# Kernel optimization log

Measured on AMD Instinct MI355X. Metric: run time of the kernel, lower is better.

Reference implementation:

```python
import jax, jax.numpy as jnp
import numpy as np

N_NODES = 100000
N_EDGES = 3200000
D_FEAT = 256
UNITS = 256


def setup_inputs() -> dict:
    key = jax.random.key(0)
    k1, k2, k3, k4, k5 = jax.random.split(key, 5)
    X = jax.random.normal(k1, (N_NODES, D_FEAT), dtype=jnp.float32)
    edge_row = jax.random.randint(k2, (N_EDGES,), 0, N_NODES, dtype=jnp.int64 if jax.config.read('jax_enable_x64') else jnp.int32)
    edge_col = jax.random.randint(k3, (N_EDGES,), 0, N_NODES, dtype=edge_row.dtype)
    edge_val = jax.random.uniform(k4, (N_EDGES,), dtype=jnp.float32)
    W = jax.random.normal(k5, (D_FEAT, UNITS), dtype=jnp.float32) * (1.0 / np.sqrt(D_FEAT))
    b = jnp.zeros((UNITS,), dtype=jnp.float32)
    return {"X": X, "edge_row": edge_row, "edge_col": edge_col,
            "edge_val": edge_val, "W": W, "b": b}


def reference(X, edge_row, edge_col, edge_val, W, b):
    # h = X @ W  (dense GEMM)  [N, units]
    h = X @ W
    # out = A @ h (sparse COO SpMM): out[i] = sum_e val[e] * h[col[e]] for row[e]==i
    msgs = edge_val[:, None] * h[edge_col]          # [E, units] gather + scale
    out = jax.ops.segment_sum(msgs, edge_row, num_segments=X.shape[0])
    out = out + b                                    # bias_add
    return jax.nn.relu(out)                          # activation
```

## Files before the change

kernel.cpp:

```cpp
#include <hip/hip_runtime.h>
#include <hip/hip_bf16.h>

#define N_NODES 100000
#define N_EDGES 3200000
#define D_FEAT  256
#define UNITS   256

#define BROWS   128
#define NB      782
#define NCHUNK  512
#define EPB     (N_EDGES / NCHUNK)
#define MAXB    6144
#define KPT     (MAXB / 512)
#define GEMMB   ((N_NODES + 127) / 128)

using frag_ab = __attribute__((ext_vector_type(8))) short;
using frag_cd = __attribute__((ext_vector_type(4))) float;

__device__ __forceinline__ unsigned short f2bf(float f) {
    union { float f; unsigned int i; } c; c.f = f;
    unsigned int r = c.i + 0x7FFF + ((c.i >> 16) & 1);
    return (unsigned short)(r >> 16);
}

__global__ __launch_bounds__(256) void convert_wt(const float* __restrict__ W,
                                                  unsigned short* __restrict__ Wt) {
    const int n = blockIdx.x, k = threadIdx.x;
    Wt[n * 256 + k] = f2bf(W[k * 256 + n]);
}

__global__ __launch_bounds__(512) void gemm_hist(const float* __restrict__ X,
                                                 const unsigned short* __restrict__ Wt,
                                                 unsigned char* __restrict__ hq,
                                                 float* __restrict__ hscale,
                                                 const int* __restrict__ erow,
                                                 int* __restrict__ hist_g) {
    __shared__ __align__(16) unsigned char smem[32768];
    __shared__ int rowmax_i[128];
    const int t = threadIdx.x;

    if (blockIdx.x >= GEMMB) {
        int* h = (int*)smem;
        const int b = blockIdx.x - GEMMB;
        for (int i = t; i < NB; i += 512) h[i] = 0;
        __syncthreads();
        const int base_e = b * EPB;
        for (int i = t; i < EPB; i += 512)
            atomicAdd(&h[erow[base_e + i] >> 7], 1);
        __syncthreads();
        for (int i = t; i < NB; i += 512)
            hist_g[b * NB + i] = h[i];
        return;
    }

    unsigned short* As = (unsigned short*)smem;
    unsigned short* Bs = (unsigned short*)(smem + 8192);
    unsigned char*  qbuf = smem;

    const int lane = t & 63;
    const int wave = t >> 6;
    const int wm   = (wave >> 2) * 64;
    const int wn   = (wave & 3) * 64;
    const int rowBase = blockIdx.x * 128;
    const int lr = lane & 15, lq = lane >> 4;

    if (t < 128) rowmax_i[t] = 0;

    frag_cd acc[4][4];
    #pragma unroll
    for (int i = 0; i < 4; ++i)
        #pragma unroll
        for (int j = 0; j < 4; ++j)
            acc[i][j] = (frag_cd){0.f, 0.f, 0.f, 0.f};

    for (int k0 = 0; k0 < D_FEAT; k0 += 32) {
        #pragma unroll
        for (int cc = 0; cc < 2; ++cc) {
            const int c = t + cc * 512;
            const int r = c >> 3, fo = (c & 7) * 4;
            const int grow = min(rowBase + r, N_NODES - 1);
            const float4 xv = *(const float4*)(X + (size_t)grow * D_FEAT + k0 + fo);
            ushort4 o;
            o.x = f2bf(xv.x); o.y = f2bf(xv.y); o.z = f2bf(xv.z); o.w = f2bf(xv.w);
            *(ushort4*)(As + r * 32 + fo) = o;
        }
        #pragma unroll
        for (int cc = 0; cc < 2; ++cc) {
            const int c = t + cc * 512;
            *(uint4*)(Bs + c * 8) =
                *(const uint4*)(Wt + (size_t)(c >> 2) * 256 + k0 + (c & 3) * 8);
        }
        __syncthreads();

        frag_ab a[4], b[4];
        #pragma unroll
        for (int i = 0; i < 4; ++i)
            a[i] = *(const frag_ab*)(As + (wm + i * 16 + lr) * 32 + lq * 8);
        #pragma unroll
        for (int j = 0; j < 4; ++j)
            b[j] = *(const frag_ab*)(Bs + (wn + j * 16 + lr) * 32 + lq * 8);

        #pragma unroll
        for (int i = 0; i < 4; ++i)
            #pragma unroll
            for (int j = 0; j < 4; ++j)
                acc[i][j] = __builtin_amdgcn_mfma_f32_16x16x32_bf16(
                    a[i], b[j], acc[i][j], 0, 0, 0);
        __syncthreads();
    }

    float pm[4][4];
    #pragma unroll
    for (int i = 0; i < 4; ++i)
        #pragma unroll
        for (int rr = 0; rr < 4; ++rr) {
            float m = fabsf(acc[i][0][rr]);
            m = fmaxf(m, fabsf(acc[i][1][rr]));
            m = fmaxf(m, fabsf(acc[i][2][rr]));
            m = fmaxf(m, fabsf(acc[i][3][rr]));
            pm[i][rr] = m;
        }
    #pragma unroll
    for (int o = 1; o <= 8; o <<= 1)
        #pragma unroll
        for (int i = 0; i < 4; ++i)
            #pragma unroll
            for (int rr = 0; rr < 4; ++rr)
                pm[i][rr] = fmaxf(pm[i][rr], __shfl_xor(pm[i][rr], o));
    if (lr == 0) {
        #pragma unroll
        for (int i = 0; i < 4; ++i)
            #pragma unroll
            for (int rr = 0; rr < 4; ++rr)
                atomicMax(&rowmax_i[wm + i * 16 + lq * 4 + rr],
                          __float_as_int(pm[i][rr]));
    }
    __syncthreads();

    #pragma unroll
    for (int i = 0; i < 4; ++i)
        #pragma unroll
        for (int rr = 0; rr < 4; ++rr) {
            const int row = wm + i * 16 + lq * 4 + rr;
            const float m = __int_as_float(rowmax_i[row]);
            const float inv = (m > 0.f) ? 127.f / m : 0.f;
            #pragma unroll
            for (int j = 0; j < 4; ++j) {
                const int q = (int)rintf(acc[i][j][rr] * inv);
                qbuf[row * 256 + wn + j * 16 + lr] = (unsigned char)(signed char)q;
            }
        }
    __syncthreads();

    #pragma unroll
    for (int cc = 0; cc < 4; ++cc) {
        const int c = t + cc * 512;
        const int row = c >> 4, fo = (c & 15) * 16;
        const int grow = rowBase + row;
        if (grow < N_NODES)
            *(uint4*)(hq + (size_t)grow * 256 + fo) = *(const uint4*)(qbuf + row * 256 + fo);
    }
    if (t < 128 && rowBase + t < N_NODES)
        hscale[rowBase + t] = __int_as_float(rowmax_i[t]) * (1.f / 127.f);
}

__global__ __launch_bounds__(512) void scan_buckets(const int* __restrict__ hist_g,
                                                    int* __restrict__ cum,
                                                    int* __restrict__ total) {
    const int k = blockIdx.x, t = threadIdx.x;
    __shared__ int p[512];
    const int v = hist_g[t * NB + k];
    p[t] = v;
    __syncthreads();
    for (int d = 1; d < 512; d <<= 1) {
        const int u = (t >= d) ? p[t - d] : 0;
        __syncthreads();
        p[t] += u;
        __syncthreads();
    }
    cum[t * NB + k] = p[t] - v;
    if (t == 511) total[k] = p[511];
}

__global__ __launch_bounds__(1024) void scan_base(const int* __restrict__ total,
                                                  int* __restrict__ base) {
    const int t = threadIdx.x;
    __shared__ int p[1024];
    const int v = (t < NB) ? total[t] : 0;
    p[t] = v;
    __syncthreads();
    for (int d = 1; d < 1024; d <<= 1) {
        const int u = (t >= d) ? p[t - d] : 0;
        __syncthreads();
        p[t] += u;
        __syncthreads();
    }
    if (t < NB) base[t] = p[t] - v;
    if (t == NB - 1) base[NB] = p[t];
}

__global__ __launch_bounds__(512) void scatter_binned(const int* __restrict__ erow,
                                                      const int* __restrict__ ecol,
                                                      const float* __restrict__ eval,
                                                      const float* __restrict__ hscale,
                                                      const int* __restrict__ cum,
                                                      const int* __restrict__ base,
                                                      uint2* __restrict__ binned) {
    __shared__ int cur[NB];
    const int t = threadIdx.x;
    const int b = blockIdx.x;
    for (int i = t; i < NB; i += 512)
        cur[i] = base[i] + cum[b * NB + i];
    __syncthreads();
    const int base_e = b * EPB;
    for (int i = t; i < EPB; i += 512) {
        const int e = base_e + i;
        const int r = erow[e];
        const int c = ecol[e];
        const float v = eval[e] * hscale[c];
        const int k = r >> 7, rl = r & 127;
        const int pos = atomicAdd(&cur[k], 1);
        binned[pos] = make_uint2(((unsigned)rl << 17) | (unsigned)c,
                                 __float_as_uint(v));
    }
}

__global__ __launch_bounds__(512) void sort_local(const uint2* __restrict__ binned,
                                                  const int* __restrict__ base,
                                                  const int* __restrict__ total,
                                                  uint2* __restrict__ sorted,
                                                  int* __restrict__ offs) {
    __shared__ uint2 buf[MAXB];
    __shared__ int lh[BROWS], loff[BROWS], lcur[BROWS];
    const int k = blockIdx.x, t = threadIdx.x;
    const int s = base[k];
    const int cnt = min(total[k], MAXB);

    uint2 ed[KPT];
    #pragma unroll
    for (int kk = 0; kk < KPT; ++kk) {
        const int i = t + kk * 512;
        if (i < cnt) ed[kk] = binned[s + i];
    }

    if (t < BROWS) lh[t] = 0;
    __syncthreads();
    #pragma unroll
    for (int kk = 0; kk < KPT; ++kk)
        if (t + kk * 512 < cnt)
            atomicAdd(&lh[ed[kk].x >> 17], 1);
    __syncthreads();
    if (t < BROWS) loff[t] = lh[t];
    __syncthreads();
    for (int d = 1; d < BROWS; d <<= 1) {
        const int u = (t >= d && t < BROWS) ? loff[t - d] : 0;
        __syncthreads();
        if (t < BROWS) loff[t] += u;
        __syncthreads();
    }
    if (t < BROWS) lcur[t] = loff[t] - lh[t];
    __syncthreads();
    #pragma unroll
    for (int kk = 0; kk < KPT; ++kk) {
        if (t + kk * 512 < cnt) {
            const int rl = ed[kk].x >> 17;
            const int p = atomicAdd(&lcur[rl], 1);
            buf[p] = make_uint2(ed[kk].x & 0x1FFFF, ed[kk].y);
        }
    }
    __syncthreads();
    for (int i = t; i < cnt; i += 512)
        sorted[s + i] = buf[i];
    const int rowBase = k * BROWS;
    if (t < BROWS && rowBase + t < N_NODES)
        offs[rowBase + t] = s + (loff[t] - lh[t]);
    if (t == 0 && k == NB - 1)
        offs[N_NODES] = N_EDGES;
}

__global__ __launch_bounds__(64) void spmm_rows(const int* __restrict__ offs,
                                                const uint2* __restrict__ sorted,
                                                const unsigned char* __restrict__ hq,
                                                const float* __restrict__ bias,
                                                float* __restrict__ out) {
    const int r = blockIdx.x;
    const int lane = threadIdx.x;
    __shared__ uint2 le[64];
    int s = offs[r];
    const int e = offs[r + 1];
    float a0 = 0.f, a1 = 0.f, a2 = 0.f, a3 = 0.f;

    while (s < e) {
        const int cnt = min(64, e - s);
        if (lane < cnt) {
            uint2 v = sorted[s + lane];
            v.x &= 0x1FFFF;
            le[lane] = v;
        }
        __syncthreads();
        #pragma unroll 4
        for (int j = 0; j < cnt; ++j) {
            const uint2 cv = le[j];
            const float v = __uint_as_float(cv.y);
            const unsigned int w = *(const unsigned int*)(hq + (size_t)cv.x * 256 + lane * 4);
            a0 += v * (float)((int)(signed char)( w        & 0xFF));
            a1 += v * (float)((int)(signed char)((w >> 8)  & 0xFF));
            a2 += v * (float)((int)(signed char)((w >> 16) & 0xFF));
            a3 += v * (float)((int)(signed char)( w >> 24        ));
        }
        __syncthreads();
        s += cnt;
    }

    const float4 b4 = *(const float4*)(bias + lane * 4);
    float4 o;
    o.x = fmaxf(a0 + b4.x, 0.f);
    o.y = fmaxf(a1 + b4.y, 0.f);
    o.z = fmaxf(a2 + b4.z, 0.f);
    o.w = fmaxf(a3 + b4.w, 0.f);
    *(float4*)(out + (size_t)r * 256 + lane * 4) = o;
}

extern "C" void kernel_launch(void* const* d_in, const int* in_sizes, int n_in,
                              void* d_out, int out_size, void* d_ws, size_t ws_size,
                              hipStream_t stream) {
    const float* X    = (const float*)d_in[0];
    const int*   erow = (const int*)  d_in[1];
    const int*   ecol = (const int*)  d_in[2];
    const float* evalv= (const float*)d_in[3];
    const float* W    = (const float*)d_in[4];
    const float* bias = (const float*)d_in[5];
    float* out = (float*)d_out;

    char* ws = (char*)d_ws;
    size_t off = 0;
    auto alloc = [&](size_t bytes) {
        void* p = ws + off;
        off += (bytes + 255) & ~(size_t)255;
        return p;
    };
    unsigned short* Wt     = (unsigned short*)alloc((size_t)D_FEAT * UNITS * 2);
    unsigned char*  hq     = (unsigned char*) alloc((size_t)N_NODES * UNITS);
    float*          hscale = (float*)         alloc((size_t)N_NODES * 4);
    uint2*          binned = (uint2*)         alloc((size_t)N_EDGES * 8);
    uint2*          sorted = (uint2*)         alloc((size_t)N_EDGES * 8);
    int*            hist_g = (int*)           alloc((size_t)NCHUNK * NB * 4);
    int*            cum    = (int*)           alloc((size_t)NCHUNK * NB * 4);
    int*            total  = (int*)           alloc((size_t)NB * 4);
    int*            basep  = (int*)           alloc((size_t)(NB + 1) * 4);
    int*            offs   = (int*)           alloc((size_t)(N_NODES + 1) * 4);

    convert_wt<<<UNITS, 256, 0, stream>>>(W, Wt);
    gemm_hist<<<GEMMB + NCHUNK, 512, 0, stream>>>(X, Wt, hq, hscale, erow, hist_g);
    scan_buckets<<<NB, 512, 0, stream>>>(hist_g, cum, total);
    scan_base<<<1, 1024, 0, stream>>>(total, basep);
    scatter_binned<<<NCHUNK, 512, 0, stream>>>(erow, ecol, evalv, hscale, cum, basep, binned);
    sort_local<<<NB, 512, 0, stream>>>(binned, basep, total, sorted, offs);
    spmm_rows<<<N_NODES, 64, 0, stream>>>(offs, sorted, hq, bias, out);
}
```

Before: 434.8 us.

## Replace scan-based bucketing with fixed-capacity buckets and global atomic cursors

Removes the histogram/scan pipeline (two scan kernels, convert_wt kernel, global hist and cum arrays) and instead gives each 128-row bucket a fixed slot of MAXB entries. Each scatter block builds a local histogram and reserves space through padded global atomic cursors. Sort writes back in place and emits per-bucket offsets, and the W transpose/convert is folded into the GEMM tile load. This cuts kernel launches and global memory traffic, but it assumes no bucket exceeds MAXB edges, makes edge order within a bucket nondeterministic, and adds strided LDS stores when loading W.

Measured after the change: 502.7 us. 1.16x slower.

```diff
diff --git a/kernel.cpp b/kernel.cpp
--- a/kernel.cpp
+++ b/kernel.cpp
@@ -12,6 +12,7 @@
 #define EPB     (N_EDGES / NCHUNK)
 #define MAXB    6144
 #define KPT     (MAXB / 512)
+#define GSTR    16
 #define GEMMB   ((N_NODES + 127) / 128)
 
 using frag_ab = __attribute__((ext_vector_type(8))) short;
@@ -23,33 +24,17 @@
     return (unsigned short)(r >> 16);
 }
 
-__global__ __launch_bounds__(256) void convert_wt(const float* __restrict__ W,
-                                                  unsigned short* __restrict__ Wt) {
-    const int n = blockIdx.x, k = threadIdx.x;
-    Wt[n * 256 + k] = f2bf(W[k * 256 + n]);
-}
-
-__global__ __launch_bounds__(512) void gemm_hist(const float* __restrict__ X,
-                                                 const unsigned short* __restrict__ Wt,
-                                                 unsigned char* __restrict__ hq,
-                                                 float* __restrict__ hscale,
-                                                 const int* __restrict__ erow,
-                                                 int* __restrict__ hist_g) {
+__global__ __launch_bounds__(512) void gemm_q(const float* __restrict__ X,
+                                              const float* __restrict__ W,
+                                              unsigned char* __restrict__ hq,
+                                              float* __restrict__ hscale,
+                                              int* __restrict__ gcur) {
     __shared__ __align__(16) unsigned char smem[32768];
     __shared__ int rowmax_i[128];
     const int t = threadIdx.x;
 
     if (blockIdx.x >= GEMMB) {
-        int* h = (int*)smem;
-        const int b = blockIdx.x - GEMMB;
-        for (int i = t; i < NB; i += 512) h[i] = 0;
-        __syncthreads();
-        const int base_e = b * EPB;
-        for (int i = t; i < EPB; i += 512)
-            atomicAdd(&h[erow[base_e + i] >> 7], 1);
-        __syncthreads();
-        for (int i = t; i < NB; i += 512)
-            hist_g[b * NB + i] = h[i];
+        for (int i = t; i < NB; i += 512) gcur[i * GSTR] = i * MAXB;
         return;
     }
 
@@ -72,6 +57,8 @@
         #pragma unroll
         for (int j = 0; j < 4; ++j)
             acc[i][j] = (frag_cd){0.f, 0.f, 0.f, 0.f};
+
+    const int wk = t >> 4, nb = (t & 15) * 16;
 
     for (int k0 = 0; k0 < D_FEAT; k0 += 32) {
         #pragma unroll
@@ -84,11 +71,28 @@
             o.x = f2bf(xv.x); o.y = f2bf(xv.y); o.z = f2bf(xv.z); o.w = f2bf(xv.w);
             *(ushort4*)(As + r * 32 + fo) = o;
         }
-        #pragma unroll
-        for (int cc = 0; cc < 2; ++cc) {
-            const int c = t + cc * 512;
-            *(uint4*)(Bs + c * 8) =
-                *(const uint4*)(Wt + (size_t)(c >> 2) * 256 + k0 + (c & 3) * 8);
+        {
+            const float* wr = W + (size_t)(k0 + wk) * 256 + nb;
+            const float4 w0 = *(const float4*)(wr + 0);
+            const float4 w1 = *(const float4*)(wr + 4);
+            const float4 w2 = *(const float4*)(wr + 8);
+            const float4 w3 = *(const float4*)(wr + 12);
+            Bs[(nb +  0) * 32 + wk] = f2bf(w0.x);
+            Bs[(nb +  1) * 32 + wk] = f2bf(w0.y);
+            Bs[(nb +  2) * 32 + wk] = f2bf(w0.z);
+            Bs[(nb +  3) * 32 + wk] = f2bf(w0.w);
+            Bs[(nb +  4) * 32 + wk] = f2bf(w1.x);
+            Bs[(nb +  5) * 32 + wk] = f2bf(w1.y);
+            Bs[(nb +  6) * 32 + wk] = f2bf(w1.z);
+            Bs[(nb +  7) * 32 + wk] = f2bf(w1.w);
+            Bs[(nb +  8) * 32 + wk] = f2bf(w2.x);
+            Bs[(nb +  9) * 32 + wk] = f2bf(w2.y);
+            Bs[(nb + 10) * 32 + wk] = f2bf(w2.z);
+            Bs[(nb + 11) * 32 + wk] = f2bf(w2.w);
+            Bs[(nb + 12) * 32 + wk] = f2bf(w3.x);
+            Bs[(nb + 13) * 32 + wk] = f2bf(w3.y);
+            Bs[(nb + 14) * 32 + wk] = f2bf(w3.z);
+            Bs[(nb + 15) * 32 + wk] = f2bf(w3.w);
         }
         __syncthreads();
 
@@ -164,55 +168,26 @@
         hscale[rowBase + t] = __int_as_float(rowmax_i[t]) * (1.f / 127.f);
 }
 
-__global__ __launch_bounds__(512) void scan_buckets(const int* __restrict__ hist_g,
-                                                    int* __restrict__ cum,
-                                                    int* __restrict__ total) {
-    const int k = blockIdx.x, t = threadIdx.x;
-    __shared__ int p[512];
-    const int v = hist_g[t * NB + k];
-    p[t] = v;
-    __syncthreads();
-    for (int d = 1; d < 512; d <<= 1) {
-        const int u = (t >= d) ? p[t - d] : 0;
-        __syncthreads();
-        p[t] += u;
-        __syncthreads();
-    }
-    cum[t * NB + k] = p[t] - v;
-    if (t == 511) total[k] = p[511];
-}
-
-__global__ __launch_bounds__(1024) void scan_base(const int* __restrict__ total,
-                                                  int* __restrict__ base) {
-    const int t = threadIdx.x;
-    __shared__ int p[1024];
-    const int v = (t < NB) ? total[t] : 0;
-    p[t] = v;
-    __syncthreads();
-    for (int d = 1; d < 1024; d <<= 1) {
-        const int u = (t >= d) ? p[t - d] : 0;
-        __syncthreads();
-        p[t] += u;
-        __syncthreads();
-    }
-    if (t < NB) base[t] = p[t] - v;
-    if (t == NB - 1) base[NB] = p[t];
-}
-
-__global__ __launch_bounds__(512) void scatter_binned(const int* __restrict__ erow,
-                                                      const int* __restrict__ ecol,
-                                                      const float* __restrict__ eval,
-                                                      const float* __restrict__ hscale,
-                                                      const int* __restrict__ cum,
-                                                      const int* __restrict__ base,
-                                                      uint2* __restrict__ binned) {
-    __shared__ int cur[NB];
+__global__ __launch_bounds__(512) void scatter_fused(const int* __restrict__ erow,
+                                                     const int* __restrict__ ecol,
+                                                     const float* __restrict__ eval,
+                                                     const float* __restrict__ hscale,
+                                                     int* __restrict__ gcur,
+                                                     uint2* __restrict__ binned) {
+    __shared__ int h[NB], cur[NB];
     const int t = threadIdx.x;
     const int b = blockIdx.x;
-    for (int i = t; i < NB; i += 512)
-        cur[i] = base[i] + cum[b * NB + i];
+    for (int i = t; i < NB; i += 512) h[i] = 0;
     __syncthreads();
     const int base_e = b * EPB;
+    for (int i = t; i < EPB; i += 512)
+        atomicAdd(&h[erow[base_e + i] >> 7], 1);
+    __syncthreads();
+    for (int k = t; k < NB; k += 512) {
+        const int c = h[k];
+        cur[k] = c ? atomicAdd(&gcur[k * GSTR], c) : 0;
+    }
+    __syncthreads();
     for (int i = t; i < EPB; i += 512) {
         const int e = base_e + i;
         const int r = erow[e];
@@ -225,16 +200,14 @@
     }
 }
 
-__global__ __launch_bounds__(512) void sort_local(const uint2* __restrict__ binned,
-                                                  const int* __restrict__ base,
-                                                  const int* __restrict__ total,
-                                                  uint2* __restrict__ sorted,
-                                                  int* __restrict__ offs) {
+__global__ __launch_bounds__(512) void sort_local(uint2* __restrict__ binned,
+                                                  const int* __restrict__ gcur,
+                                                  int* __restrict__ offs2) {
     __shared__ uint2 buf[MAXB];
     __shared__ int lh[BROWS], loff[BROWS], lcur[BROWS];
     const int k = blockIdx.x, t = threadIdx.x;
-    const int s = base[k];
-    const int cnt = min(total[k], MAXB);
+    const int s = k * MAXB;
+    const int cnt = min(gcur[k * GSTR] - s, MAXB);
 
     uint2 ed[KPT];
     #pragma unroll
@@ -270,30 +243,30 @@
     }
     __syncthreads();
     for (int i = t; i < cnt; i += 512)
-        sorted[s + i] = buf[i];
-    const int rowBase = k * BROWS;
-    if (t < BROWS && rowBase + t < N_NODES)
-        offs[rowBase + t] = s + (loff[t] - lh[t]);
-    if (t == 0 && k == NB - 1)
-        offs[N_NODES] = N_EDGES;
-}
-
-__global__ __launch_bounds__(64) void spmm_rows(const int* __restrict__ offs,
-                                                const uint2* __restrict__ sorted,
+        binned[s + i] = buf[i];
+    if (t < BROWS)
+        offs2[k * 129 + t] = s + (loff[t] - lh[t]);
+    if (t == 128)
+        offs2[k * 129 + 128] = s + cnt;
+}
+
+__global__ __launch_bounds__(64) void spmm_rows(const int* __restrict__ offs2,
+                                                const uint2* __restrict__ binned,
                                                 const unsigned char* __restrict__ hq,
                                                 const float* __restrict__ bias,
                                                 float* __restrict__ out) {
     const int r = blockIdx.x;
     const int lane = threadIdx.x;
     __shared__ uint2 le[64];
-    int s = offs[r];
-    const int e = offs[r + 1];
+    const int kb = (r >> 7) * 129 + (r & 127);
+    int s = offs2[kb];
+    const int e = offs2[kb + 1];
     float a0 = 0.f, a1 = 0.f, a2 = 0.f, a3 = 0.f;
 
     while (s < e) {
         const int cnt = min(64, e - s);
         if (lane < cnt) {
-            uint2 v = sorted[s + lane];
+            uint2 v = binned[s + lane];
             v.x &= 0x1FFFF;
             le[lane] = v;
         }
@@ -339,22 +312,14 @@
         off += (bytes + 255) & ~(size_t)255;
         return p;
     };
-    unsigned short* Wt     = (unsigned short*)alloc((size_t)D_FEAT * UNITS * 2);
-    unsigned char*  hq     = (unsigned char*) alloc((size_t)N_NODES * UNITS);
-    float*          hscale = (float*)         alloc((size_t)N_NODES * 4);
-    uint2*          binned = (uint2*)         alloc((size_t)N_EDGES * 8);
-    uint2*          sorted = (uint2*)         alloc((size_t)N_EDGES * 8);
-    int*            hist_g = (int*)           alloc((size_t)NCHUNK * NB * 4);
-    int*            cum    = (int*)           alloc((size_t)NCHUNK * NB * 4);
-    int*            total  = (int*)           alloc((size_t)NB * 4);
-    int*            basep  = (int*)           alloc((size_t)(NB + 1) * 4);
-    int*            offs   = (int*)           alloc((size_t)(N_NODES + 1) * 4);
-
-    convert_wt<<<UNITS, 256, 0, stream>>>(W, Wt);
-    gemm_hist<<<GEMMB + NCHUNK, 512, 0, stream>>>(X, Wt, hq, hscale, erow, hist_g);
-    scan_buckets<<<NB, 512, 0, stream>>>(hist_g, cum, total);
-    scan_base<<<1, 1024, 0, stream>>>(total, basep);
-    scatter_binned<<<NCHUNK, 512, 0, stream>>>(erow, ecol, evalv, hscale, cum, basep, binned);
-    sort_local<<<NB, 512, 0, stream>>>(binned, basep, total, sorted, offs);
-    spmm_rows<<<N_NODES, 64, 0, stream>>>(offs, sorted, hq, bias, out);
-}
+    unsigned char* hq     = (unsigned char*)alloc((size_t)N_NODES * UNITS);
+    float*         hscale = (float*)        alloc((size_t)N_NODES * 4);
+    uint2*         binned = (uint2*)        alloc((size_t)NB * MAXB * 8);
+    int*           gcur   = (int*)          alloc((size_t)NB * GSTR * 4);
+    int*           offs2  = (int*)          alloc((size_t)NB * 129 * 4);
+
+    gemm_q<<<GEMMB + 1, 512, 0, stream>>>(X, W, hq, hscale, gcur);
+    scatter_fused<<<NCHUNK, 512, 0, stream>>>(erow, ecol, evalv, hscale, gcur, binned);
+    sort_local<<<NB, 512, 0, stream>>>(binned, gcur, offs2);
+    spmm_rows<<<N_NODES, 64, 0, stream>>>(offs2, binned, hq, bias, out);
+}
```
